# Optimization experiments

Hardware: AMD Instinct MI355X
Metric: run time of the kernel (lower is better)

## Reference

```python
import jax, jax.numpy as jnp
import numpy as np
import math

B, T, C, D = 8, 2048, 1024, 1024
N_LAYER, LAYER_ID = 24, 12


def setup_inputs() -> dict:
    key = jax.random.key(0)
    ks = jax.random.split(key, 5)
    r01 = LAYER_ID / (N_LAYER - 1)
    r10 = 1.0 - LAYER_ID / N_LAYER
    ddd = np.arange(C, dtype=np.float64) / C                      # (C,)
    h = np.arange(D, dtype=np.float64)
    decay_speed = -5 + 8 * (h / (D - 1)) ** (0.7 + 1.3 * r01)     # time_decay init
    zigzag = ((np.arange(D) + 1) % 3 - 1) * 0.5
    time_first = np.log(0.3) + zigzag
    scale = C ** -0.5
    return {
        "x": jax.random.normal(ks[0], (B, T, C), jnp.float32),
        "time_decay": jnp.asarray(decay_speed, jnp.float32),
        "time_first": jnp.asarray(time_first, jnp.float32),
        "time_mix_k": jnp.asarray(ddd ** r10, jnp.float32),
        "time_mix_v": jnp.asarray(ddd ** r10 + 0.3 * r01, jnp.float32),
        "time_mix_r": jnp.asarray(ddd ** (0.5 * r10), jnp.float32),
        "Wk": jax.random.normal(ks[1], (D, C), jnp.float32) * scale,
        "Wv": jax.random.normal(ks[2], (D, C), jnp.float32) * scale,
        "Wr": jax.random.normal(ks[3], (D, C), jnp.float32) * scale,
        "Wo": jax.random.normal(ks[4], (C, D), jnp.float32) * scale,
    }


def _wkv(time_decay, time_first, k, v):
    # wkv_t = (e^{u+k_t} v_t + A_{t-1}) / (e^{u+k_t} + B_{t-1})
    # A_t = e^w A_{t-1} + e^{k_t} v_t ;  B_t likewise with v=1 ;  w = -exp(time_decay)
    # Exactly the math of the original conv1d-with-exp-curve trick, in O(T).
    ew = jnp.exp(-jnp.exp(time_decay))   # (D,)
    eu = jnp.exp(time_first)             # (D,)
    ek = jnp.exp(k)                      # [B,T,D]
    ekv = ek * v

    def step(carry, inp):
        a, b = carry                     # [B,D] each
        ekt, ekvt = inp                  # [B,D] each
        out = (eu * ekvt + a) / (eu * ekt + b)
        return (ew * a + ekvt, ew * b + ekt), out

    init = (jnp.zeros_like(ek[:, 0]), jnp.zeros_like(ek[:, 0]))
    xs = (jnp.swapaxes(ek, 0, 1), jnp.swapaxes(ekv, 0, 1))  # [T,B,D]
    _, out = jax.lax.scan(step, init, xs)
    return jnp.swapaxes(out, 0, 1)       # [B,T,D]


def reference(x, time_decay, time_first, time_mix_k, time_mix_v, time_mix_r, Wk, Wv, Wr, Wo):
    # time_shift: prepend zero row, drop last (ZeroPad2d((0,0,1,-1)))
    xx = jnp.pad(x, ((0, 0), (1, 0), (0, 0)))[:, :-1]
    xk = x * time_mix_k + xx * (1 - time_mix_k)
    xv = x * time_mix_v + xx * (1 - time_mix_v)
    xr = x * time_mix_r + xx * (1 - time_mix_r)
    k = jnp.einsum('btc,dc->btd', xk, Wk)
    v = jnp.einsum('btc,dc->btd', xv, Wv)
    sr = jax.nn.sigmoid(jnp.einsum('btc,dc->btd', xr, Wr))
    rwkv = sr * _wkv(time_decay, time_first, k, v)
    return jnp.einsum('btd,cd->btc', rwkv, Wo)
```

## Files before the change

### kernel.cpp

```cpp
#include <hip/hip_runtime.h>
#include <cstdint>
#include <cstddef>

#define Bb 8
#define Tt 2048
#define Cc 1024
#define Dd 1024
#define Mm (Bb*Tt)
#define CL 64
#define NCH (Tt/CL)


typedef __bf16  bf16x8  __attribute__((ext_vector_type(8)));
typedef float   floatx4 __attribute__((ext_vector_type(4)));

__device__ __forceinline__ ushort f2bf(float f) {
    unsigned u = __float_as_uint(f);
    u = (u + 0x7FFF + ((u >> 16) & 1)) >> 16;
    return (ushort)u;
}
__device__ __forceinline__ float bf2f(ushort u) {
    return __uint_as_float(((unsigned)u) << 16);
}

__device__ __forceinline__ void load_lds16(const void* g, void* l) {
    __builtin_amdgcn_global_load_lds((__attribute__((address_space(1))) void*)(g),
                                     (__attribute__((address_space(3))) void*)(l),
                                     16, 0, 0);
}

__global__ __launch_bounds__(256) void prep_mix3(
        const float* __restrict__ x,
        const float* __restrict__ mk, const float* __restrict__ mv,
        const float* __restrict__ mr,
        ushort* __restrict__ xk, ushort* __restrict__ xv, ushort* __restrict__ xr) {
    int i  = blockIdx.x * 256 + threadIdx.x;
    int cq = i & (Cc / 8 - 1);
    int m  = i >> 7;
    int t  = m & (Tt - 1);
    float xc[8], xp[8];
    *(float4*)&xc[0] = ((const float4*)x)[i * 2];
    *(float4*)&xc[4] = ((const float4*)x)[i * 2 + 1];
    if (t != 0) {
        *(float4*)&xp[0] = ((const float4*)x)[(i - Cc / 8) * 2];
        *(float4*)&xp[4] = ((const float4*)x)[(i - Cc / 8) * 2 + 1];
    } else {
#pragma unroll
        for (int j = 0; j < 8; j++) xp[j] = 0.f;
    }
    float wk[8], wv[8], wr[8];
    *(float4*)&wk[0] = ((const float4*)mk)[cq * 2];
    *(float4*)&wk[4] = ((const float4*)mk)[cq * 2 + 1];
    *(float4*)&wv[0] = ((const float4*)mv)[cq * 2];
    *(float4*)&wv[4] = ((const float4*)mv)[cq * 2 + 1];
    *(float4*)&wr[0] = ((const float4*)mr)[cq * 2];
    *(float4*)&wr[4] = ((const float4*)mr)[cq * 2 + 1];
    ushort ok[8], ov[8], orr[8];
#pragma unroll
    for (int j = 0; j < 8; j++) {
        float d = xc[j] - xp[j];
        ok[j]  = f2bf(xp[j] + d * wk[j]);
        ov[j]  = f2bf(xp[j] + d * wv[j]);
        orr[j] = f2bf(xp[j] + d * wr[j]);
    }
    ((ulonglong2*)xk)[i] = *(const ulonglong2*)ok;
    ((ulonglong2*)xv)[i] = *(const ulonglong2*)ov;
    ((ulonglong2*)xr)[i] = *(const ulonglong2*)orr;
}

__global__ __launch_bounds__(256) void cvt_w(
        const float* __restrict__ wk, const float* __restrict__ wv,
        const float* __restrict__ wr, const float* __restrict__ wo,
        ushort* __restrict__ ok, ushort* __restrict__ ov,
        ushort* __restrict__ orr, ushort* __restrict__ oo) {
    int i = blockIdx.x * 256 + threadIdx.x;
    int sel = i >> 18;
    int j = i & ((1 << 18) - 1);
    const float* s = sel == 0 ? wk : sel == 1 ? wv : sel == 2 ? wr : wo;
    ushort* d      = sel == 0 ? ok : sel == 1 ? ov : sel == 2 ? orr : oo;
    float4 f = ((const float4*)s)[j];
    ushort4 o;
    o.x = f2bf(f.x); o.y = f2bf(f.y); o.z = f2bf(f.z); o.w = f2bf(f.w);
    ((ushort4*)d)[j] = o;
}

template<int MODE>
__global__ __launch_bounds__(256) void gemm_nt(
        const ushort* __restrict__ A, const ushort* __restrict__ Bw,
        void* __restrict__ Co, int Ndim, int Kdim) {
    __shared__ __attribute__((aligned(16))) __bf16 As[128 * 32];
    __shared__ __attribute__((aligned(16))) __bf16 Bs[128 * 32];
    const int tid  = threadIdx.x;
    const int lane = tid & 63;
    const int quad = lane >> 4;
    const int fr   = lane & 15;
    const int wave = tid >> 6;
    const int wm   = (wave >> 1) * 64;
    const int wn   = (wave & 1) * 64;
    const long tm  = (long)blockIdx.x * 128;
    const long tn  = (long)blockIdx.y * 128;

    const int srow  = tid >> 2;
    const int spart = (tid & 3) ^ ((tid >> 3) & 3);
    const ushort* Ag0 = A + (tm + srow) * (long)Kdim + spart * 8;
    const ushort* Ag1 = Ag0 + 64 * (long)Kdim;
    const ushort* Bg0 = Bw + (tn + srow) * (long)Kdim + spart * 8;
    const ushort* Bg1 = Bg0 + 64 * (long)Kdim;
    __bf16* AlA = &As[wave * 512];
    __bf16* AlB = &As[2048 + wave * 512];
    __bf16* BlA = &Bs[wave * 512];
    __bf16* BlB = &Bs[2048 + wave * 512];

    const int swz = (fr >> 1) & 3;

    floatx4 zero = {0.f, 0.f, 0.f, 0.f};
    floatx4 acc[4][4];
#pragma unroll
    for (int a1 = 0; a1 < 4; a1++)
#pragma unroll
        for (int b1 = 0; b1 < 4; b1++) acc[a1][b1] = zero;

    for (int kt = 0; kt < Kdim; kt += 32) {
        __syncthreads();
        load_lds16(Ag0 + kt, AlA);
        load_lds16(Ag1 + kt, AlB);
        load_lds16(Bg0 + kt, BlA);
        load_lds16(Bg1 + kt, BlB);
        __syncthreads();

        bf16x8 af[4], bfg[4];
#pragma unroll
        for (int mi = 0; mi < 4; mi++)
            af[mi] = *(const bf16x8*)&As[(wm + mi * 16 + fr) * 32 + (quad ^ swz) * 8];
#pragma unroll
        for (int ni = 0; ni < 4; ni++)
            bfg[ni] = *(const bf16x8*)&Bs[(wn + ni * 16 + fr) * 32 + (quad ^ swz) * 8];
#pragma unroll
        for (int mi = 0; mi < 4; mi++)
#pragma unroll
            for (int ni = 0; ni < 4; ni++)
                acc[mi][ni] = __builtin_amdgcn_mfma_f32_16x16x32_bf16(
                    af[mi], bfg[ni], acc[mi][ni], 0, 0, 0);
    }

#pragma unroll
    for (int mi = 0; mi < 4; mi++)
#pragma unroll
        for (int ni = 0; ni < 4; ni++)
#pragma unroll
            for (int r = 0; r < 4; r++) {
                long grow = tm + wm + mi * 16 + quad * 4 + r;
                long gcol = tn + wn + ni * 16 + fr;
                float v = acc[mi][ni][r];
                if (MODE == 2) v = 1.f / (1.f + __expf(-v));
                if (MODE == 0)      ((float*)Co)[grow * Ndim + gcol] = v;
                else if (MODE == 3) ((_Float16*)Co)[grow * Ndim + gcol] = (_Float16)v;
                else                ((ushort*)Co)[grow * Ndim + gcol] = f2bf(v);
            }
}

__global__ __launch_bounds__(256) void wkv_part(
        const _Float16* __restrict__ kb, const ushort* __restrict__ vb,
        const float* __restrict__ decay,
        float* __restrict__ pa, float* __restrict__ pb) {
    int gid = blockIdx.x * 256 + threadIdx.x;
    int d = gid & (Dd - 1);
    int c = (gid >> 10) & (NCH - 1);
    int b = gid >> 15;
    float ew = __expf(-__expf(decay[d]));
    size_t base = ((size_t)b * Tt + (size_t)c * CL) * Dd + d;
    float a = 0.f, bs = 0.f;
    for (int i0 = 0; i0 < CL; i0 += 8) {
        float kr[8], vr[8];
#pragma unroll
        for (int j = 0; j < 8; j++) {
            size_t idx = base + (size_t)(i0 + j) * Dd;
            kr[j] = (float)kb[idx]; vr[j] = bf2f(vb[idx]);
        }
#pragma unroll
        for (int j = 0; j < 8; j++) {
            float ek = __expf(kr[j]);
            a  = ew * a  + ek * vr[j];
            bs = ew * bs + ek;
        }
    }
    int sidx = c * (Bb * Dd) + b * Dd + d;
    pa[sidx] = a; pb[sidx] = bs;
}

__global__ __launch_bounds__(256) void wkv_prefix(
        const float* __restrict__ pa, const float* __restrict__ pb,
        const float* __restrict__ decay,
        float* __restrict__ sa, float* __restrict__ sb) {
    int gid = blockIdx.x * 256 + threadIdx.x;
    int d = gid & (Dd - 1);
    float ewL = __expf(-__expf(decay[d]) * (float)CL);
    float ca = 0.f, cb = 0.f;
#pragma unroll
    for (int c = 0; c < NCH; c++) {
        int idx = c * (Bb * Dd) + gid;
        sa[idx] = ca; sb[idx] = cb;
        ca = ewL * ca + pa[idx];
        cb = ewL * cb + pb[idx];
    }
}

__global__ __launch_bounds__(256) void wkv_chunk(
        const _Float16* __restrict__ kb, const ushort* __restrict__ vb,
        const ushort* __restrict__ sr,
        const float* __restrict__ decay, const float* __restrict__ tf,
        const float* __restrict__ sa, const float* __restrict__ sb,
        ushort* __restrict__ rw) {
    int gid = blockIdx.x * 256 + threadIdx.x;
    int d = gid & (Dd - 1);
    int c = (gid >> 10) & (NCH - 1);
    int b = gid >> 15;
    float ew = __expf(-__expf(decay[d]));
    float eu = __expf(tf[d]);
    int sidx = c * (Bb * Dd) + b * Dd + d;
    float a = sa[sidx], bs = sb[sidx];
    size_t base = ((size_t)b * Tt + (size_t)c * CL) * Dd + d;
    for (int i0 = 0; i0 < CL; i0 += 8) {
        float kr[8], vr[8], rr[8];
#pragma unroll
        for (int j = 0; j < 8; j++) {
            size_t idx = base + (size_t)(i0 + j) * Dd;
            kr[j] = (float)kb[idx]; vr[j] = bf2f(vb[idx]); rr[j] = bf2f(sr[idx]);
        }
#pragma unroll
        for (int j = 0; j < 8; j++) {
            float ek  = __expf(kr[j]);
            float ekv = ek * vr[j];
            float out = (eu * ekv + a) / (eu * ek + bs);
            a  = ew * a  + ekv;
            bs = ew * bs + ek;
            rw[base + (size_t)(i0 + j) * Dd] = f2bf(rr[j] * out);
        }
    }
}

extern "C" void kernel_launch(void* const* d_in, const int* in_sizes, int n_in,
                              void* d_out, int out_size, void* d_ws, size_t ws_size,
                              hipStream_t stream) {
    (void)in_sizes; (void)n_in; (void)out_size; (void)ws_size;
    const float* x  = (const float*)d_in[0];
    const float* td = (const float*)d_in[1];
    const float* tf = (const float*)d_in[2];
    const float* mk = (const float*)d_in[3];
    const float* mv = (const float*)d_in[4];
    const float* mr = (const float*)d_in[5];
    const float* Wk = (const float*)d_in[6];
    const float* Wv = (const float*)d_in[7];
    const float* Wr = (const float*)d_in[8];
    const float* Wo = (const float*)d_in[9];
    float* out = (float*)d_out;

    char* p = (char*)d_ws;
    auto take = [&](size_t n) { char* r = p; p += n; return r; };
    ushort*   xk = (ushort*)take((size_t)Mm * Cc * 2);
    ushort*   xv = (ushort*)take((size_t)Mm * Cc * 2);
    ushort*   xr = (ushort*)take((size_t)Mm * Cc * 2);
    _Float16* kb = (_Float16*)take((size_t)Mm * Dd * 2);
    ushort*   wk = (ushort*)take((size_t)Dd * Cc * 2);
    ushort*   wv = (ushort*)take((size_t)Dd * Cc * 2);
    ushort*   wr = (ushort*)take((size_t)Dd * Cc * 2);
    ushort*   wo = (ushort*)take((size_t)Cc * Dd * 2);
    float*    pa = (float*)take((size_t)Bb * NCH * Dd * 4);
    float*    pb = (float*)take((size_t)Bb * NCH * Dd * 4);
    float*    sa = (float*)take((size_t)Bb * NCH * Dd * 4);
    float*    sbst = (float*)take((size_t)Bb * NCH * Dd * 4);
    ushort*   vb = xk;
    ushort*   sb = xv;
    ushort*   rw = xr;

    dim3 g1(Mm / 128, Dd / 128);
    dim3 g2(Mm / 128, Cc / 128);
    const int wkv_grid = (Bb * NCH * Dd) / 256;

    cvt_w<<<4096, 256, 0, stream>>>(Wk, Wv, Wr, Wo, wk, wv, wr, wo);
    prep_mix3<<<Mm * Cc / 8 / 256, 256, 0, stream>>>(x, mk, mv, mr, xk, xv, xr);

    gemm_nt<3><<<g1, 256, 0, stream>>>(xk, wk, kb, Dd, Cc);
    gemm_nt<1><<<g1, 256, 0, stream>>>(xv, wv, vb, Dd, Cc);
    gemm_nt<2><<<g1, 256, 0, stream>>>(xr, wr, sb, Dd, Cc);

    wkv_part  <<<wkv_grid, 256, 0, stream>>>(kb, vb, td, pa, pb);
    wkv_prefix<<<(Bb * Dd) / 256, 256, 0, stream>>>(pa, pb, td, sa, sbst);
    wkv_chunk <<<wkv_grid, 256, 0, stream>>>(kb, vb, sb, td, tf, sa, sbst, rw);

    gemm_nt<0><<<g2, 256, 0, stream>>>(rw, wo, out, Cc, Dd);
}
```

Baseline: 421.7 us.

## Double-buffer GEMM LDS tiles and merge K/V/R projections into one launch

Each GEMM tile loop now double-buffers its LDS tiles, prefetching the next K slice while computing the current one, which removes one barrier per iteration. The three projection GEMMs are fused into a single launch, with the projection chosen per block. This fused path only runs if the workspace holds separate v and sr buffers, and otherwise falls back to the original three launches. The change doubles LDS use per block, which may lower occupancy, and it depends on the harness giving a larger workspace.

```diff
diff --git a/kernel.cpp b/kernel.cpp
--- a/kernel.cpp
+++ b/kernel.cpp
@@ -84,78 +84,128 @@
     ((ushort4*)d)[j] = o;
 }
 
+struct GemmCore {
+    floatx4 acc[4][4];
+    int quad, fr, wave, wm, wn;
+
+    __device__ __forceinline__ void run(
+            const ushort* __restrict__ A, const ushort* __restrict__ Bw,
+            long tm, long tn, int Kdim,
+            __bf16* As, __bf16* Bs) {
+        const int tid  = threadIdx.x;
+        const int lane = tid & 63;
+        quad = lane >> 4;
+        fr   = lane & 15;
+        wave = tid >> 6;
+        wm   = (wave >> 1) * 64;
+        wn   = (wave & 1) * 64;
+
+        const int srow  = tid >> 2;
+        const int spart = (tid & 3) ^ ((tid >> 3) & 3);
+        const ushort* Ag0 = A + (tm + srow) * (long)Kdim + spart * 8;
+        const ushort* Ag1 = Ag0 + 64 * (long)Kdim;
+        const ushort* Bg0 = Bw + (tn + srow) * (long)Kdim + spart * 8;
+        const ushort* Bg1 = Bg0 + 64 * (long)Kdim;
+        const int swz = (fr >> 1) & 3;
+
+        floatx4 zero = {0.f, 0.f, 0.f, 0.f};
+#pragma unroll
+        for (int a1 = 0; a1 < 4; a1++)
+#pragma unroll
+            for (int b1 = 0; b1 < 4; b1++) acc[a1][b1] = zero;
+
+        const int niter = Kdim >> 5;
+        load_lds16(Ag0, &As[wave * 512]);
+        load_lds16(Ag1, &As[2048 + wave * 512]);
+        load_lds16(Bg0, &Bs[wave * 512]);
+        load_lds16(Bg1, &Bs[2048 + wave * 512]);
+
+        for (int it = 0; it < niter; ++it) {
+            const int cur = it & 1;
+            __bf16* Ac = As + cur * 4096;
+            __bf16* Bc = Bs + cur * 4096;
+            __syncthreads();
+            if (it + 1 < niter) {
+                const int kt = (it + 1) << 5;
+                __bf16* An = As + (cur ^ 1) * 4096;
+                __bf16* Bn = Bs + (cur ^ 1) * 4096;
+                load_lds16(Ag0 + kt, &An[wave * 512]);
+                load_lds16(Ag1 + kt, &An[2048 + wave * 512]);
+                load_lds16(Bg0 + kt, &Bn[wave * 512]);
+                load_lds16(Bg1 + kt, &Bn[2048 + wave * 512]);
+            }
+            bf16x8 af[4], bfg[4];
+#pragma unroll
+            for (int mi = 0; mi < 4; mi++)
+                af[mi] = *(const bf16x8*)&Ac[(wm + mi * 16 + fr) * 32 + (quad ^ swz) * 8];
+#pragma unroll
+            for (int ni = 0; ni < 4; ni++)
+                bfg[ni] = *(const bf16x8*)&Bc[(wn + ni * 16 + fr) * 32 + (quad ^ swz) * 8];
+#pragma unroll
+            for (int mi = 0; mi < 4; mi++)
+#pragma unroll
+                for (int ni = 0; ni < 4; ni++)
+                    acc[mi][ni] = __builtin_amdgcn_mfma_f32_16x16x32_bf16(
+                        af[mi], bfg[ni], acc[mi][ni], 0, 0, 0);
+        }
+    }
+};
+
 template<int MODE>
 __global__ __launch_bounds__(256) void gemm_nt(
         const ushort* __restrict__ A, const ushort* __restrict__ Bw,
         void* __restrict__ Co, int Ndim, int Kdim) {
-    __shared__ __attribute__((aligned(16))) __bf16 As[128 * 32];
-    __shared__ __attribute__((aligned(16))) __bf16 Bs[128 * 32];
-    const int tid  = threadIdx.x;
-    const int lane = tid & 63;
-    const int quad = lane >> 4;
-    const int fr   = lane & 15;
-    const int wave = tid >> 6;
-    const int wm   = (wave >> 1) * 64;
-    const int wn   = (wave & 1) * 64;
-    const long tm  = (long)blockIdx.x * 128;
-    const long tn  = (long)blockIdx.y * 128;
-
-    const int srow  = tid >> 2;
-    const int spart = (tid & 3) ^ ((tid >> 3) & 3);
-    const ushort* Ag0 = A + (tm + srow) * (long)Kdim + spart * 8;
-    const ushort* Ag1 = Ag0 + 64 * (long)Kdim;
-    const ushort* Bg0 = Bw + (tn + srow) * (long)Kdim + spart * 8;
-    const ushort* Bg1 = Bg0 + 64 * (long)Kdim;
-    __bf16* AlA = &As[wave * 512];
-    __bf16* AlB = &As[2048 + wave * 512];
-    __bf16* BlA = &Bs[wave * 512];
-    __bf16* BlB = &Bs[2048 + wave * 512];
-
-    const int swz = (fr >> 1) & 3;
-
-    floatx4 zero = {0.f, 0.f, 0.f, 0.f};
-    floatx4 acc[4][4];
-#pragma unroll
-    for (int a1 = 0; a1 < 4; a1++)
-#pragma unroll
-        for (int b1 = 0; b1 < 4; b1++) acc[a1][b1] = zero;
-
-    for (int kt = 0; kt < Kdim; kt += 32) {
-        __syncthreads();
-        load_lds16(Ag0 + kt, AlA);
-        load_lds16(Ag1 + kt, AlB);
-        load_lds16(Bg0 + kt, BlA);
-        load_lds16(Bg1 + kt, BlB);
-        __syncthreads();
-
-        bf16x8 af[4], bfg[4];
-#pragma unroll
-        for (int mi = 0; mi < 4; mi++)
-            af[mi] = *(const bf16x8*)&As[(wm + mi * 16 + fr) * 32 + (quad ^ swz) * 8];
+    __shared__ __attribute__((aligned(16))) __bf16 As[2 * 128 * 32];
+    __shared__ __attribute__((aligned(16))) __bf16 Bs[2 * 128 * 32];
+    const long tm = (long)blockIdx.x * 128;
+    const long tn = (long)blockIdx.y * 128;
+    GemmCore g;
+    g.run(A, Bw, tm, tn, Kdim, As, Bs);
+#pragma unroll
+    for (int mi = 0; mi < 4; mi++)
 #pragma unroll
         for (int ni = 0; ni < 4; ni++)
-            bfg[ni] = *(const bf16x8*)&Bs[(wn + ni * 16 + fr) * 32 + (quad ^ swz) * 8];
-#pragma unroll
-        for (int mi = 0; mi < 4; mi++)
-#pragma unroll
-            for (int ni = 0; ni < 4; ni++)
-                acc[mi][ni] = __builtin_amdgcn_mfma_f32_16x16x32_bf16(
-                    af[mi], bfg[ni], acc[mi][ni], 0, 0, 0);
-    }
-
-#pragma unroll
-    for (int mi = 0; mi < 4; mi++)
-#pragma unroll
-        for (int ni = 0; ni < 4; ni++)
 #pragma unroll
             for (int r = 0; r < 4; r++) {
-                long grow = tm + wm + mi * 16 + quad * 4 + r;
-                long gcol = tn + wn + ni * 16 + fr;
-                float v = acc[mi][ni][r];
+                long grow = tm + g.wm + mi * 16 + g.quad * 4 + r;
+                long gcol = tn + g.wn + ni * 16 + g.fr;
+                float v = g.acc[mi][ni][r];
                 if (MODE == 2) v = 1.f / (1.f + __expf(-v));
                 if (MODE == 0)      ((float*)Co)[grow * Ndim + gcol] = v;
                 else if (MODE == 3) ((_Float16*)Co)[grow * Ndim + gcol] = (_Float16)v;
                 else                ((ushort*)Co)[grow * Ndim + gcol] = f2bf(v);
+            }
+}
+
+__global__ __launch_bounds__(256) void gemm3_nt(
+        const ushort* __restrict__ xk, const ushort* __restrict__ xv,
+        const ushort* __restrict__ xr,
+        const ushort* __restrict__ wk, const ushort* __restrict__ wv,
+        const ushort* __restrict__ wr,
+        _Float16* __restrict__ kb, ushort* __restrict__ vb,
+        ushort* __restrict__ sb) {
+    __shared__ __attribute__((aligned(16))) __bf16 As[2 * 128 * 32];
+    __shared__ __attribute__((aligned(16))) __bf16 Bs[2 * 128 * 32];
+    const int proj = blockIdx.y >> 3;
+    const long tm = (long)blockIdx.x * 128;
+    const long tn = (long)(blockIdx.y & 7) * 128;
+    const ushort* A  = proj == 0 ? xk : proj == 1 ? xv : xr;
+    const ushort* Bw = proj == 0 ? wk : proj == 1 ? wv : wr;
+    GemmCore g;
+    g.run(A, Bw, tm, tn, Cc, As, Bs);
+#pragma unroll
+    for (int mi = 0; mi < 4; mi++)
+#pragma unroll
+        for (int ni = 0; ni < 4; ni++)
+#pragma unroll
+            for (int r = 0; r < 4; r++) {
+                long grow = tm + g.wm + mi * 16 + g.quad * 4 + r;
+                long gcol = tn + g.wn + ni * 16 + g.fr;
+                long off = grow * Dd + gcol;
+                float v = g.acc[mi][ni][r];
+                if (proj == 0)      kb[off] = (_Float16)v;
+                else if (proj == 1) vb[off] = f2bf(v);
+                else                sb[off] = f2bf(1.f / (1.f + __expf(-v)));
             }
 }
 
@@ -242,7 +292,7 @@
 extern "C" void kernel_launch(void* const* d_in, const int* in_sizes, int n_in,
                               void* d_out, int out_size, void* d_ws, size_t ws_size,
                               hipStream_t stream) {
-    (void)in_sizes; (void)n_in; (void)out_size; (void)ws_size;
+    (void)in_sizes; (void)n_in; (void)out_size;
     const float* x  = (const float*)d_in[0];
     const float* td = (const float*)d_in[1];
     const float* tf = (const float*)d_in[2];
@@ -255,34 +305,52 @@
     const float* Wo = (const float*)d_in[9];
     float* out = (float*)d_out;
 
+    const size_t xsz = (size_t)Mm * Cc * 2;
+    const size_t wsz = (size_t)Dd * Cc * 2;
+    const size_t ssz = (size_t)Bb * NCH * Dd * 4;
+    const size_t need_merged = 6 * xsz + 4 * wsz + 4 * ssz;
+
     char* p = (char*)d_ws;
     auto take = [&](size_t n) { char* r = p; p += n; return r; };
-    ushort*   xk = (ushort*)take((size_t)Mm * Cc * 2);
-    ushort*   xv = (ushort*)take((size_t)Mm * Cc * 2);
-    ushort*   xr = (ushort*)take((size_t)Mm * Cc * 2);
-    _Float16* kb = (_Float16*)take((size_t)Mm * Dd * 2);
-    ushort*   wk = (ushort*)take((size_t)Dd * Cc * 2);
-    ushort*   wv = (ushort*)take((size_t)Dd * Cc * 2);
-    ushort*   wr = (ushort*)take((size_t)Dd * Cc * 2);
-    ushort*   wo = (ushort*)take((size_t)Cc * Dd * 2);
-    float*    pa = (float*)take((size_t)Bb * NCH * Dd * 4);
-    float*    pb = (float*)take((size_t)Bb * NCH * Dd * 4);
-    float*    sa = (float*)take((size_t)Bb * NCH * Dd * 4);
-    float*    sbst = (float*)take((size_t)Bb * NCH * Dd * 4);
-    ushort*   vb = xk;
-    ushort*   sb = xv;
-    ushort*   rw = xr;
+    ushort*   xk = (ushort*)take(xsz);
+    ushort*   xv = (ushort*)take(xsz);
+    ushort*   xr = (ushort*)take(xsz);
+    _Float16* kb = (_Float16*)take(xsz);
+    const bool merged = ws_size >= need_merged;
+    ushort *vb, *sb, *rw;
+    if (merged) {
+        vb = (ushort*)take(xsz);
+        sb = (ushort*)take(xsz);
+        rw = xk;
+    } else {
+        vb = xk;
+        sb = xv;
+        rw = xr;
+    }
+    ushort* wk = (ushort*)take(wsz);
+    ushort* wv = (ushort*)take(wsz);
+    ushort* wr = (ushort*)take(wsz);
+    ushort* wo = (ushort*)take(wsz);
+    float*  pa = (float*)take(ssz);
+    float*  pb = (float*)take(ssz);
+    float*  sa = (float*)take(ssz);
+    float*  sbst = (float*)take(ssz);
 
     dim3 g1(Mm / 128, Dd / 128);
     dim3 g2(Mm / 128, Cc / 128);
+    dim3 g3(Mm / 128, 3 * Dd / 128);
     const int wkv_grid = (Bb * NCH * Dd) / 256;
 
     cvt_w<<<4096, 256, 0, stream>>>(Wk, Wv, Wr, Wo, wk, wv, wr, wo);
     prep_mix3<<<Mm * Cc / 8 / 256, 256, 0, stream>>>(x, mk, mv, mr, xk, xv, xr);
 
-    gemm_nt<3><<<g1, 256, 0, stream>>>(xk, wk, kb, Dd, Cc);
-    gemm_nt<1><<<g1, 256, 0, stream>>>(xv, wv, vb, Dd, Cc);
-    gemm_nt<2><<<g1, 256, 0, stream>>>(xr, wr, sb, Dd, Cc);
+    if (merged) {
+        gemm3_nt<<<g3, 256, 0, stream>>>(xk, xv, xr, wk, wv, wr, kb, vb, sb);
+    } else {
+        gemm_nt<3><<<g1, 256, 0, stream>>>(xk, wk, kb, Dd, Cc);
+        gemm_nt<1><<<g1, 256, 0, stream>>>(xv, wv, vb, Dd, Cc);
+        gemm_nt<2><<<g1, 256, 0, stream>>>(xr, wr, sb, Dd, Cc);
+    }
 
     wkv_part  <<<wkv_grid, 256, 0, stream>>>(kb, vb, td, pa, pb);
     wkv_prefix<<<(Bb * Dd) / 256, 256, 0, stream>>>(pa, pb, td, sa, sbst);
```

New measurement: 408.0 us. -3.3%, faster.
